# Kernel optimization log

Measured on AMD Instinct MI355X. Metric: run time of the kernel, lower is better.

## Reference

```python
import jax, jax.numpy as jnp
import numpy as np

D = 256   # input_size
H = 512   # hidden_size
A = 4     # alpha_dim
K = 2 * A * A  # output values per input dim (binary=False -> 2 params)


def _masks():
    # MADE sequential-ordering masks, per DART.create_masks
    in_deg = np.arange(D)
    hid_deg = np.arange(H) % (D - 1)
    out_deg = np.arange(D) - 1  # arange(D) % D - 1
    m0 = (hid_deg[:, None] >= in_deg[None, :]).astype(np.float32)   # [H, D]
    mh = (hid_deg[:, None] >= hid_deg[None, :]).astype(np.float32)  # [H, H]
    ml = (out_deg[:, None] >= hid_deg[None, :]).astype(np.float32)  # [D, H]
    # repeat(1, K).view(-1, H): each output-dim row repeated K consecutive times
    ml = np.repeat(ml, K, axis=0)                                    # [D*K, H]
    return jnp.asarray(m0), jnp.asarray(mh), jnp.asarray(ml)


def setup_inputs() -> dict:
    key = jax.random.key(0)
    ks = jax.random.split(key, 10)
    B = 1024
    x = jax.random.normal(ks[0], (B, D), dtype=jnp.float32)
    def lin(k, out_dim, in_dim):
        s = 1.0 / np.sqrt(in_dim)
        kw, kb = jax.random.split(k)
        W = jax.random.uniform(kw, (out_dim, in_dim), jnp.float32, -s, s)
        b = jax.random.uniform(kb, (out_dim,), jnp.float32, -s, s)
        return W, b
    W0, b0 = lin(ks[1], H, D)
    W1, b1 = lin(ks[2], H, H)
    W2, b2 = lin(ks[3], H, H)
    Wout, bout = lin(ks[4], D * K, H)
    # unnormalized_log_p_alpha initialized to log(1/A)
    ulpa = jnp.full((1, D - 1, 1, A), -np.log(A), dtype=jnp.float32)
    return {"x": x, "W0": W0, "b0": b0, "W1": W1, "b1": b1,
            "W2": W2, "b2": b2, "Wout": Wout, "bout": bout, "ulpa": ulpa}


def reference(x, W0, b0, W1, b1, W2, b2, Wout, bout, ulpa):
    m0, mh, ml = _masks()
    B = x.shape[0]
    # masked MLP (MADE)
    h = jax.nn.relu(x @ (m0 * W0).T + b0)
    h = jax.nn.relu(h @ (mh * W1).T + b1)
    h = jax.nn.relu(h @ (mh * W2).T + b2)
    theta = (h @ (ml * Wout).T + bout).reshape(B, D, 2, A, A)
    mu = theta[:, :, 0]                      # [B, D, A, A]
    std = jnp.exp(theta[:, :, 1]) + 0.01     # [B, D, A, A]
    xe = x[:, :, None, None]
    # Normal log-prob
    log_px = -0.5 * jnp.square((xe - mu) / std) - jnp.log(std) - 0.5 * jnp.log(2.0 * jnp.pi)
    # normalized log p(alpha): [1, D-1, 1, A]
    lpa = jax.nn.log_softmax(ulpa, axis=-1)
    joint = log_px[:, :-1] + lpa             # [B, D-1, A, A]
    first = joint[:, 0, 0:1]                 # [B, 1, A]
    inner = jnp.swapaxes(joint[:, 1:], 0, 1)  # [D-2, B, A, A]
    # HMM-style forward recursion: stable log-domain chain matmul via scan
    def step(carry, m):
        # carry: [B, 1, A]; m: [B, A, A]
        new = jax.nn.logsumexp(carry[:, :, :, None] + m[:, None, :, :], axis=-2)
        return new, None
    carry, _ = jax.lax.scan(step, first, inner)
    last = log_px[:, -1, :, 0:1]             # [B, A, 1]
    log_p = jax.nn.logsumexp(carry[:, :, :, None] + last[:, None, :, :], axis=-2)  # [B,1,1]
    return log_p, theta
```

## Files before the change

### kernel.cpp

```cpp
#include <hip/hip_runtime.h>
#include <math.h>

#define Bsz 1024
#define Dd  256
#define Hh  512
#define NOUT 8192

typedef __attribute__((ext_vector_type(8))) short bf8_t;
typedef __attribute__((ext_vector_type(4))) float f4_t;

__device__ inline ushort f2b(float f) {
  union { float f; unsigned u; } c; c.f = f;
  unsigned r = c.u + 0x7fffu + ((c.u >> 16) & 1u);
  return (ushort)(r >> 16);
}

__device__ inline void async16(const ushort* g, ushort* l) {
  __builtin_amdgcn_global_load_lds((const __attribute__((address_space(1))) void*)g,
                                   (__attribute__((address_space(3))) void*)l, 16, 0, 0);
}

__device__ inline int mod255(int v) {
  if (v >= 510) return v - 510;
  if (v >= 255) return v - 255;
  return v;
}

__global__ __launch_bounds__(256) void prep(
    const float* __restrict__ x,  const float* __restrict__ W0,
    const float* __restrict__ W1, const float* __restrict__ W2,
    const float* __restrict__ Wout, const float* __restrict__ ulpa,
    ushort* __restrict__ xb, ushort* __restrict__ w0b, ushort* __restrict__ w1b,
    ushort* __restrict__ w2b, ushort* __restrict__ woutb,
    float* __restrict__ lpa)
{
  const int blk = blockIdx.x, tid = threadIdx.x;
  if (blk == 2496) {
    if (tid < Dd - 1) {
      float v0 = ulpa[tid * 4 + 0], v1 = ulpa[tid * 4 + 1];
      float v2 = ulpa[tid * 4 + 2], v3 = ulpa[tid * 4 + 3];
      float m = fmaxf(fmaxf(v0, v1), fmaxf(v2, v3));
      float s = __expf(v0 - m) + __expf(v1 - m) + __expf(v2 - m) + __expf(v3 - m);
      float l = m + __logf(s);
      lpa[tid * 4 + 0] = v0 - l;
      lpa[tid * 4 + 1] = v1 - l;
      lpa[tid * 4 + 2] = v2 - l;
      lpa[tid * 4 + 3] = v3 - l;
    }
    return;
  }
  const float* src; ushort* dst; int lb, mode;
  if (blk < 128)      { src = x;    dst = xb;    lb = blk;       mode = 0; }
  else if (blk < 192) { src = W0;   dst = w0b;   lb = blk - 128; mode = 1; }
  else if (blk < 320) { src = W1;   dst = w1b;   lb = blk - 192; mode = 2; }
  else if (blk < 448) { src = W2;   dst = w2b;   lb = blk - 320; mode = 2; }
  else                { src = Wout; dst = woutb; lb = blk - 448; mode = 3; }

  const int e = lb * 2048 + tid * 8;
  float4 v0 = *(const float4*)(src + e);
  float4 v1 = *(const float4*)(src + e + 4);
  float vv[8] = {v0.x, v0.y, v0.z, v0.w, v1.x, v1.y, v1.z, v1.w};
  ushort u[8];
  if (mode == 0) {
#pragma unroll
    for (int i = 0; i < 8; i++) u[i] = f2b(vv[i]);
  } else if (mode == 1) {
    int n = e >> 8, k0 = e & 255, nd = mod255(n);
#pragma unroll
    for (int i = 0; i < 8; i++) u[i] = (nd >= k0 + i) ? f2b(vv[i]) : (ushort)0;
  } else if (mode == 2) {
    int n = e >> 9, k0 = e & 511, nd = mod255(n);
#pragma unroll
    for (int i = 0; i < 8; i++) u[i] = (nd >= mod255(k0 + i)) ? f2b(vv[i]) : (ushort)0;
  } else {
    int n = e >> 9, k0 = e & 511, nd = (n >> 5) - 1;
#pragma unroll
    for (int i = 0; i < 8; i++) u[i] = (nd >= mod255(k0 + i)) ? f2b(vv[i]) : (ushort)0;
  }
  *(ushort4*)(dst + e)     = *(ushort4*)&u[0];
  *(ushort4*)(dst + e + 4) = *(ushort4*)&u[4];
}

template<int KD>
__global__ __launch_bounds__(256) void gemm_s(
    const ushort* __restrict__ A, const ushort* __restrict__ W,
    const float* __restrict__ bias, ushort* __restrict__ Ch)
{
  constexpr int NT = KD / 64;
  __shared__ ushort As[3][64 * 64];
  __shared__ ushort Bs[3][32 * 64];
  const int tid = threadIdx.x, lane = tid & 63, wave = tid >> 6;
  const int row0 = blockIdx.y * 64, col0 = blockIdx.x * 32;
  const int fm = lane & 15, qq = lane >> 4;
  const int srow = lane >> 3, qslot = lane & 7;

  f4_t acc[2];
  acc[0] = (f4_t){0.f, 0.f, 0.f, 0.f};
  acc[1] = (f4_t){0.f, 0.f, 0.f, 0.f};

  auto stage = [&](int buf, int kt) {
#pragma unroll
    for (int a = 0; a < 2; a++) {
      int rb = wave * 16 + a * 8;
      int r = rb + srow;
      int q = (qslot - r) & 7;
      async16(A + (size_t)(row0 + r) * KD + kt + q * 8, &As[buf][rb * 64]);
    }
    {
      int rb = wave * 8;
      int r = rb + srow;
      int q = (qslot - r) & 7;
      async16(W + (size_t)(col0 + r) * KD + kt + q * 8, &Bs[buf][rb * 64]);
    }
  };

  stage(0, 0);
  stage(1, 64);

#pragma unroll
  for (int i = 0; i < NT; i++) {
    if (i + 1 < NT) asm volatile("s_waitcnt vmcnt(3)" ::: "memory");
    else            asm volatile("s_waitcnt vmcnt(0)" ::: "memory");
    __builtin_amdgcn_s_barrier();
    asm volatile("" ::: "memory");
    if (i + 2 < NT) stage((i + 2) % 3, (i + 2) * 64);
    const int buf = i % 3;
#pragma unroll
    for (int t = 0; t < 2; t++) {
      int ra = wave * 16 + fm;
      int slota = ((t * 4 + qq) + ra) & 7;
      bf8_t af = *(const bf8_t*)&As[buf][ra * 64 + slota * 8];
#pragma unroll
      for (int j = 0; j < 2; j++) {
        int rb = j * 16 + fm;
        int slot = ((t * 4 + qq) + rb) & 7;
        bf8_t bf = *(const bf8_t*)&Bs[buf][rb * 64 + slot * 8];
        acc[j] = __builtin_amdgcn_mfma_f32_16x16x32_bf16(af, bf, acc[j], 0, 0, 0);
      }
    }
    asm volatile("s_waitcnt lgkmcnt(0)" ::: "memory");
  }

#pragma unroll
  for (int j = 0; j < 2; j++) {
    int col = col0 + j * 16 + fm;
    float bv = bias[col];
    int rbase = row0 + wave * 16 + qq * 4;
#pragma unroll
    for (int r = 0; r < 4; r++) {
      float t = fmaxf(acc[j][r] + bv, 0.0f);
      Ch[(size_t)(rbase + r) * Hh + col] = f2b(t);
    }
  }
}

__global__ __launch_bounds__(256) void gemm_big(
    const ushort* __restrict__ A, const ushort* __restrict__ W,
    const float* __restrict__ bias, float* __restrict__ Cf,
    int M, int N, int Kd)
{
  __shared__ ushort As[2][128 * 64];
  __shared__ ushort Bs[2][128 * 64];
  const int tid = threadIdx.x, lane = tid & 63, wave = tid >> 6;
  const int waveM = wave >> 1, waveN = wave & 1;
  const int row0 = blockIdx.y * 128, col0 = blockIdx.x * 128;
  const int fm = lane & 15, qq = lane >> 4;
  const int srow = lane >> 3, qslot = lane & 7;

  f4_t acc[4][4];
#pragma unroll
  for (int i = 0; i < 4; i++)
#pragma unroll
    for (int j = 0; j < 4; j++) acc[i][j] = (f4_t){0.f, 0.f, 0.f, 0.f};

  auto stage = [&](int buf, int kt) {
#pragma unroll
    for (int p = 0; p < 4; p++) {
      int rb = p * 32 + wave * 8;
      int r = rb + srow;
      int q = (qslot - r) & 7;
      async16(A + (size_t)(row0 + r) * Kd + kt + q * 8, &As[buf][rb * 64]);
    }
#pragma unroll
    for (int p = 0; p < 4; p++) {
      int rb = p * 32 + wave * 8;
      int r = rb + srow;
      int q = (qslot - r) & 7;
      async16(W + (size_t)(col0 + r) * Kd + kt + q * 8, &Bs[buf][rb * 64]);
    }
  };

  stage(0, 0);
  int cur = 0;
  for (int kt = 0; kt < Kd; kt += 64) {
    asm volatile("s_waitcnt vmcnt(0)" ::: "memory");
    __builtin_amdgcn_s_barrier();
    asm volatile("" ::: "memory");
    if (kt + 64 < Kd) stage(cur ^ 1, kt + 64);
#pragma unroll
    for (int t = 0; t < 2; t++) {
      bf8_t af[4], bf[4];
#pragma unroll
      for (int i = 0; i < 4; i++) {
        int r = waveM * 64 + i * 16 + fm;
        int slot = ((t * 4 + qq) + r) & 7;
        af[i] = *(const bf8_t*)&As[cur][r * 64 + slot * 8];
      }
#pragma unroll
      for (int j = 0; j < 4; j++) {
        int r = waveN * 64 + j * 16 + fm;
        int slot = ((t * 4 + qq) + r) & 7;
        bf[j] = *(const bf8_t*)&Bs[cur][r * 64 + slot * 8];
      }
#pragma unroll
      for (int i = 0; i < 4; i++)
#pragma unroll
        for (int j = 0; j < 4; j++)
          acc[i][j] = __builtin_amdgcn_mfma_f32_16x16x32_bf16(af[i], bf[j], acc[i][j], 0, 0, 0);
    }
    asm volatile("s_waitcnt lgkmcnt(0)" ::: "memory");
    cur ^= 1;
  }

#pragma unroll
  for (int j = 0; j < 4; j++) {
    int col = col0 + waveN * 64 + j * 16 + fm;
    float bv = bias[col];
#pragma unroll
    for (int i = 0; i < 4; i++) {
      int rbase = row0 + waveM * 64 + i * 16 + qq * 4;
#pragma unroll
      for (int r = 0; r < 4; r++)
        Cf[(size_t)(rbase + r) * N + col] = acc[i][j][r] + bv;
    }
  }
}

__global__ __launch_bounds__(512) void chain2(
    const float* __restrict__ x, const float* __restrict__ theta,
    const float* __restrict__ lpa, float* __restrict__ logp)
{
  __shared__ float ths[256 * 33];
  __shared__ float xs[256];
  __shared__ float lps[255 * 5];
  __shared__ float TA[32][16];
  __shared__ float TB[16][16];

  const int b = blockIdx.x;
  const int tid = threadIdx.x;
  const float C0 = 0.91893853320467274178f;

  const float4* src = (const float4*)(theta + (size_t)b * NOUT);
#pragma unroll
  for (int it = 0; it < 4; it++) {
    int t = tid + it * 512;
    float4 v = src[t];
    int d = t >> 3, c = (t & 7) * 4;
    float* p = &ths[d * 33 + c];
    p[0] = v.x; p[1] = v.y; p[2] = v.z; p[3] = v.w;
  }
  if (tid < 64) ((float4*)xs)[tid] = ((const float4*)(x + (size_t)b * Dd))[tid];
  if (tid < 255) {
    float4 v = ((const float4*)lpa)[tid];
    float* p = &lps[tid * 5];
    p[0] = v.x; p[1] = v.y; p[2] = v.z; p[3] = v.w;
  }
  __syncthreads();

  const int seg = tid >> 4, e = tid & 15, ii = e >> 2, jj = e & 3;
  const int base = (tid & 63) & ~15;
  const int d0 = 1 + seg * 8;
  const int d1 = min(d0 + 8, Dd - 1);

  auto stepm = [&](int d) -> float {
    float mu = ths[d * 33 + e];
    float ls = ths[d * 33 + 16 + e];
    float s  = __expf(ls) + 0.01f;
    float z  = (xs[d] - mu) * __builtin_amdgcn_rcpf(s);
    return -0.5f * z * z - __logf(s) - C0 + lps[d * 5 + jj];
  };

  float T = stepm(d0);
  for (int d = d0 + 1; d < d1; d++) {
    float m_ = stepm(d);
    float v0 = __shfl(T, base + ii * 4 + 0) + __shfl(m_, base + 0 * 4 + jj);
    float v1 = __shfl(T, base + ii * 4 + 1) + __shfl(m_, base + 1 * 4 + jj);
    float v2 = __shfl(T, base + ii * 4 + 2) + __shfl(m_, base + 2 * 4 + jj);
    float v3 = __shfl(T, base + ii * 4 + 3) + __shfl(m_, base + 3 * 4 + jj);
    float mx = fmaxf(fmaxf(v0, v1), fmaxf(v2, v3));
    float s  = __expf(v0 - mx) + __expf(v1 - mx) + __expf(v2 - mx) + __expf(v3 - mx);
    T = mx + __logf(s);
  }
  TA[seg][e] = T;
  __syncthreads();

  float (*cur)[16] = TA;
  float (*nxt)[16] = TB;
#pragma unroll
  for (int n = 16; n >= 1; n >>= 1) {
    if (tid < n * 16) {
      int p = tid >> 4, ee = tid & 15, i2 = ee >> 2, j2 = ee & 3;
      const float* L = cur[2 * p];
      const float* R = cur[2 * p + 1];
      float v0 = L[i2 * 4 + 0] + R[0 * 4 + j2];
      float v1 = L[i2 * 4 + 1] + R[1 * 4 + j2];
      float v2 = L[i2 * 4 + 2] + R[2 * 4 + j2];
      float v3 = L[i2 * 4 + 3] + R[3 * 4 + j2];
      float mx = fmaxf(fmaxf(v0, v1), fmaxf(v2, v3));
      float ss = __expf(v0 - mx) + __expf(v1 - mx) + __expf(v2 - mx) + __expf(v3 - mx);
      nxt[p][ee] = mx + __logf(ss);
    }
    __syncthreads();
    float (*tmp)[16] = cur; cur = nxt; nxt = tmp;
  }

  if (tid < 16) {
    int i = tid >> 2, j = tid & 3;
    float mu0 = ths[i], ls0 = ths[16 + i];
    float s0 = __expf(ls0) + 0.01f;
    float z0 = (xs[0] - mu0) * __builtin_amdgcn_rcpf(s0);
    float c0 = -0.5f * z0 * z0 - __logf(s0) - C0 + lps[i];
    float muL = ths[255 * 33 + j * 4];
    float lsL = ths[255 * 33 + 16 + j * 4];
    float sL = __expf(lsL) + 0.01f;
    float zL = (xs[255] - muL) * __builtin_amdgcn_rcpf(sL);
    float lL = -0.5f * zL * zL - __logf(sL) - C0;
    float v = c0 + cur[0][tid] + lL;
    float mx = fmaxf(v, __shfl_xor(v, 1));
    mx = fmaxf(mx, __shfl_xor(mx, 2));
    mx = fmaxf(mx, __shfl_xor(mx, 4));
    mx = fmaxf(mx, __shfl_xor(mx, 8));
    float ee = __expf(v - mx);
    ee += __shfl_xor(ee, 1);
    ee += __shfl_xor(ee, 2);
    ee += __shfl_xor(ee, 4);
    ee += __shfl_xor(ee, 8);
    if (tid == 0) logp[b] = mx + __logf(ee);
  }
}

extern "C" void kernel_launch(void* const* d_in, const int* in_sizes, int n_in,
                              void* d_out, int out_size, void* d_ws, size_t ws_size,
                              hipStream_t stream)
{
  const float* x    = (const float*)d_in[0];
  const float* W0   = (const float*)d_in[1];
  const float* b0   = (const float*)d_in[2];
  const float* W1   = (const float*)d_in[3];
  const float* b1   = (const float*)d_in[4];
  const float* W2   = (const float*)d_in[5];
  const float* b2   = (const float*)d_in[6];
  const float* Wout = (const float*)d_in[7];
  const float* bout = (const float*)d_in[8];
  const float* ulpa = (const float*)d_in[9];

  float* out   = (float*)d_out;
  float* logp  = out;
  float* theta = out + Bsz;

  ushort* ws    = (ushort*)d_ws;
  ushort* xb    = ws;
  ushort* w0b   = xb + 262144;
  ushort* w1b   = w0b + 131072;
  ushort* w2b   = w1b + 262144;
  ushort* woutb = w2b + 262144;
  ushort* h0    = woutb + 4194304;
  ushort* h1    = h0 + 524288;
  ushort* h2    = h1 + 524288;
  float*  lpa   = (float*)(h2 + 524288);

  prep<<<2497, 256, 0, stream>>>(x, W0, W1, W2, Wout, ulpa,
                                 xb, w0b, w1b, w2b, woutb, lpa);
  gemm_s<Dd><<<dim3(16, 16), 256, 0, stream>>>(xb, w0b, b0, h0);
  gemm_s<Hh><<<dim3(16, 16), 256, 0, stream>>>(h0, w1b, b1, h1);
  gemm_s<Hh><<<dim3(16, 16), 256, 0, stream>>>(h1, w2b, b2, h2);
  gemm_big<<<dim3(NOUT / 128, Bsz / 128), 256, 0, stream>>>(h2, woutb, bout, theta, Bsz, NOUT, Hh);
  chain2<<<Bsz, 512, 0, stream>>>(x, theta, lpa, logp);
}
```

Measured before the change: 136.1 us.

## Fuse three hidden MLP layers into one kernel with activations kept in LDS

Replaces the three separate gemm_s launches with a single mlp3 kernel. Each of 64 blocks owns 16 batch rows, converts x to bf16 on the fly, and chains all three masked layers through swizzled shared-memory buffers. Only the final layer's activations go to global memory. This removes two kernel launches, the h0/h1 global round trips and the separate x conversion in prep. The cost is far fewer blocks (64 on a large GPU) and weights read directly from global memory without LDS staging, so each block re-reads all weight matrices.

```diff
diff --git a/kernel.cpp b/kernel.cpp
--- a/kernel.cpp
+++ b/kernel.cpp
@@ -27,15 +27,15 @@
 }
 
 __global__ __launch_bounds__(256) void prep(
-    const float* __restrict__ x,  const float* __restrict__ W0,
-    const float* __restrict__ W1, const float* __restrict__ W2,
-    const float* __restrict__ Wout, const float* __restrict__ ulpa,
-    ushort* __restrict__ xb, ushort* __restrict__ w0b, ushort* __restrict__ w1b,
+    const float* __restrict__ W0, const float* __restrict__ W1,
+    const float* __restrict__ W2, const float* __restrict__ Wout,
+    const float* __restrict__ ulpa,
+    ushort* __restrict__ w0b, ushort* __restrict__ w1b,
     ushort* __restrict__ w2b, ushort* __restrict__ woutb,
     float* __restrict__ lpa)
 {
   const int blk = blockIdx.x, tid = threadIdx.x;
-  if (blk == 2496) {
+  if (blk == 2368) {
     if (tid < Dd - 1) {
       float v0 = ulpa[tid * 4 + 0], v1 = ulpa[tid * 4 + 1];
       float v2 = ulpa[tid * 4 + 2], v3 = ulpa[tid * 4 + 3];
@@ -50,21 +50,17 @@
     return;
   }
   const float* src; ushort* dst; int lb, mode;
-  if (blk < 128)      { src = x;    dst = xb;    lb = blk;       mode = 0; }
-  else if (blk < 192) { src = W0;   dst = w0b;   lb = blk - 128; mode = 1; }
-  else if (blk < 320) { src = W1;   dst = w1b;   lb = blk - 192; mode = 2; }
-  else if (blk < 448) { src = W2;   dst = w2b;   lb = blk - 320; mode = 2; }
-  else                { src = Wout; dst = woutb; lb = blk - 448; mode = 3; }
+  if (blk < 64)       { src = W0;   dst = w0b;   lb = blk;       mode = 1; }
+  else if (blk < 192) { src = W1;   dst = w1b;   lb = blk - 64;  mode = 2; }
+  else if (blk < 320) { src = W2;   dst = w2b;   lb = blk - 192; mode = 2; }
+  else                { src = Wout; dst = woutb; lb = blk - 320; mode = 3; }
 
   const int e = lb * 2048 + tid * 8;
   float4 v0 = *(const float4*)(src + e);
   float4 v1 = *(const float4*)(src + e + 4);
   float vv[8] = {v0.x, v0.y, v0.z, v0.w, v1.x, v1.y, v1.z, v1.w};
   ushort u[8];
-  if (mode == 0) {
-#pragma unroll
-    for (int i = 0; i < 8; i++) u[i] = f2b(vv[i]);
-  } else if (mode == 1) {
+  if (mode == 1) {
     int n = e >> 8, k0 = e & 255, nd = mod255(n);
 #pragma unroll
     for (int i = 0; i < 8; i++) u[i] = (nd >= k0 + i) ? f2b(vv[i]) : (ushort)0;
@@ -81,77 +77,74 @@
   *(ushort4*)(dst + e + 4) = *(ushort4*)&u[4];
 }
 
-template<int KD>
-__global__ __launch_bounds__(256) void gemm_s(
-    const ushort* __restrict__ A, const ushort* __restrict__ W,
-    const float* __restrict__ bias, ushort* __restrict__ Ch)
-{
-  constexpr int NT = KD / 64;
-  __shared__ ushort As[3][64 * 64];
-  __shared__ ushort Bs[3][32 * 64];
+template<int KD, bool TO_GLOBAL>
+__device__ __forceinline__ void mlp_layer(
+    const ushort* hin, const ushort* __restrict__ Wg,
+    const float* __restrict__ bias, ushort* hout,
+    int row0, int lane, int wave)
+{
+  const int fm = lane & 15, qq = lane >> 4;
+#pragma unroll
+  for (int ct = 0; ct < 4; ct++) {
+    const int n0 = wave * 64 + ct * 16;
+    const ushort* wrow = Wg + (size_t)(n0 + fm) * KD;
+    f4_t acc = (f4_t){0.f, 0.f, 0.f, 0.f};
+#pragma unroll
+    for (int kt = 0; kt < KD / 64; kt++) {
+#pragma unroll
+      for (int t = 0; t < 2; t++) {
+        const int c = t * 4 + qq;
+        bf8_t af = *(const bf8_t*)&hin[(kt * 16 + fm) * 64 + ((c + fm) & 7) * 8];
+        bf8_t bf = *(const bf8_t*)(wrow + kt * 64 + c * 8);
+        acc = __builtin_amdgcn_mfma_f32_16x16x32_bf16(af, bf, acc, 0, 0, 0);
+      }
+    }
+    const int col = n0 + fm;
+    const float bv = bias[col];
+#pragma unroll
+    for (int r = 0; r < 4; r++) {
+      const int row = qq * 4 + r;
+      float tv = fmaxf(acc[r] + bv, 0.0f);
+      ushort hv = f2b(tv);
+      if (TO_GLOBAL) {
+        hout[(size_t)(row0 + row) * Hh + col] = hv;
+      } else {
+        const int kt2 = col >> 6, q2 = (col >> 3) & 7, w2 = col & 7;
+        hout[(kt2 * 16 + row) * 64 + ((q2 + row) & 7) * 8 + w2] = hv;
+      }
+    }
+  }
+}
+
+__global__ __launch_bounds__(512) void mlp3(
+    const float* __restrict__ x,
+    const ushort* __restrict__ w0b, const float* __restrict__ b0,
+    const ushort* __restrict__ w1b, const float* __restrict__ b1,
+    const ushort* __restrict__ w2b, const float* __restrict__ b2,
+    ushort* __restrict__ h2)
+{
+  __shared__ ushort hA[8 * 16 * 64];
+  __shared__ ushort hB[8 * 16 * 64];
   const int tid = threadIdx.x, lane = tid & 63, wave = tid >> 6;
-  const int row0 = blockIdx.y * 64, col0 = blockIdx.x * 32;
-  const int fm = lane & 15, qq = lane >> 4;
-  const int srow = lane >> 3, qslot = lane & 7;
-
-  f4_t acc[2];
-  acc[0] = (f4_t){0.f, 0.f, 0.f, 0.f};
-  acc[1] = (f4_t){0.f, 0.f, 0.f, 0.f};
-
-  auto stage = [&](int buf, int kt) {
-#pragma unroll
-    for (int a = 0; a < 2; a++) {
-      int rb = wave * 16 + a * 8;
-      int r = rb + srow;
-      int q = (qslot - r) & 7;
-      async16(A + (size_t)(row0 + r) * KD + kt + q * 8, &As[buf][rb * 64]);
-    }
-    {
-      int rb = wave * 8;
-      int r = rb + srow;
-      int q = (qslot - r) & 7;
-      async16(W + (size_t)(col0 + r) * KD + kt + q * 8, &Bs[buf][rb * 64]);
-    }
-  };
-
-  stage(0, 0);
-  stage(1, 64);
-
-#pragma unroll
-  for (int i = 0; i < NT; i++) {
-    if (i + 1 < NT) asm volatile("s_waitcnt vmcnt(3)" ::: "memory");
-    else            asm volatile("s_waitcnt vmcnt(0)" ::: "memory");
-    __builtin_amdgcn_s_barrier();
-    asm volatile("" ::: "memory");
-    if (i + 2 < NT) stage((i + 2) % 3, (i + 2) * 64);
-    const int buf = i % 3;
-#pragma unroll
-    for (int t = 0; t < 2; t++) {
-      int ra = wave * 16 + fm;
-      int slota = ((t * 4 + qq) + ra) & 7;
-      bf8_t af = *(const bf8_t*)&As[buf][ra * 64 + slota * 8];
-#pragma unroll
-      for (int j = 0; j < 2; j++) {
-        int rb = j * 16 + fm;
-        int slot = ((t * 4 + qq) + rb) & 7;
-        bf8_t bf = *(const bf8_t*)&Bs[buf][rb * 64 + slot * 8];
-        acc[j] = __builtin_amdgcn_mfma_f32_16x16x32_bf16(af, bf, acc[j], 0, 0, 0);
-      }
-    }
-    asm volatile("s_waitcnt lgkmcnt(0)" ::: "memory");
-  }
-
-#pragma unroll
-  for (int j = 0; j < 2; j++) {
-    int col = col0 + j * 16 + fm;
-    float bv = bias[col];
-    int rbase = row0 + wave * 16 + qq * 4;
-#pragma unroll
-    for (int r = 0; r < 4; r++) {
-      float t = fmaxf(acc[j][r] + bv, 0.0f);
-      Ch[(size_t)(rbase + r) * Hh + col] = f2b(t);
-    }
-  }
+  const int row0 = blockIdx.x * 16;
+
+#pragma unroll
+  for (int it = 0; it < 2; it++) {
+    int f = it * 512 + tid;
+    int r = f >> 6, k4 = (f & 63) << 2;
+    float4 v = *(const float4*)(x + (size_t)(row0 + r) * Dd + k4);
+    ushort4 u;
+    u.x = f2b(v.x); u.y = f2b(v.y); u.z = f2b(v.z); u.w = f2b(v.w);
+    int t = k4 >> 6, q = (k4 >> 3) & 7, half = (k4 >> 2) & 1;
+    *(ushort4*)&hA[(t * 16 + r) * 64 + ((q + r) & 7) * 8 + half * 4] = u;
+  }
+  __syncthreads();
+
+  mlp_layer<Dd, false>(hA, w0b, b0, hB, row0, lane, wave);
+  __syncthreads();
+  mlp_layer<Hh, false>(hB, w1b, b1, hA, row0, lane, wave);
+  __syncthreads();
+  mlp_layer<Hh, true >(hA, w2b, b2, h2, row0, lane, wave);
 }
 
 __global__ __launch_bounds__(256) void gemm_big(
@@ -359,21 +352,17 @@
   float* theta = out + Bsz;
 
   ushort* ws    = (ushort*)d_ws;
-  ushort* xb    = ws;
-  ushort* w0b   = xb + 262144;
+  ushort* w0b   = ws;
   ushort* w1b   = w0b + 131072;
   ushort* w2b   = w1b + 262144;
   ushort* woutb = w2b + 262144;
-  ushort* h0    = woutb + 4194304;
-  ushort* h1    = h0 + 524288;
-  ushort* h2    = h1 + 524288;
+  ushort* h2    = woutb + 4194304;
   float*  lpa   = (float*)(h2 + 524288);
 
-  prep<<<2497, 256, 0, stream>>>(x, W0, W1, W2, Wout, ulpa,
-                                 xb, w0b, w1b, w2b, woutb, lpa);
-  gemm_s<Dd><<<dim3(16, 16), 256, 0, stream>>>(xb, w0b, b0, h0);
-  gemm_s<Hh><<<dim3(16, 16), 256, 0, stream>>>(h0, w1b, b1, h1);
-  gemm_s<Hh><<<dim3(16, 16), 256, 0, stream>>>(h1, w2b, b2, h2);
-  gemm_big<<<dim3(NOUT / 128, Bsz / 128), 256, 0, stream>>>(h2, woutb, bout, theta, Bsz, NOUT, Hh);
+  prep<<<2369, 256, 0, stream>>>(W0, W1, W2, Wout, ulpa,
+                                 w0b, w1b, w2b, woutb, lpa);
+  mlp3<<<64, 512, 0, stream>>>(x, w0b, b0, w1b, b1, w2b, b2, h2);
+  gemm_big<<<dim3(NOUT / 128, Bsz / 128), 256, 0, stream>>>(
+      h2, woutb, bout, theta, Bsz, NOUT, Hh);
   chain2<<<Bsz, 512, 0, stream>>>(x, theta, lpa, logp);
 }
```

Measured after the change: 162.6 us. +19.5%, slower.

## Shrink hidden-layer GEMM tiles to 32x32 and keep log-prior in registers

Applied to the files above, without the earlier changes.

The three hidden-layer GEMMs now use 32x32 output tiles, one 16x16 MFMA tile per wave, and launch 512 blocks instead of 256 so more of the GPU's compute units are busy. The vmcnt wait is adjusted because each stage now issues one fewer async load. The chain kernel loads its slice of the normalized log-prior directly from global memory into registers, drops the LDS copy, and fully unrolls the per-segment recursion. This trades more blocks and redundant B-tile loads for more parallelism, and per-thread global loads in exchange for less LDS staging.

```diff
diff --git a/kernel.cpp b/kernel.cpp
--- a/kernel.cpp
+++ b/kernel.cpp
@@ -87,21 +87,19 @@
     const float* __restrict__ bias, ushort* __restrict__ Ch)
 {
   constexpr int NT = KD / 64;
-  __shared__ ushort As[3][64 * 64];
+  __shared__ ushort As[3][32 * 64];
   __shared__ ushort Bs[3][32 * 64];
   const int tid = threadIdx.x, lane = tid & 63, wave = tid >> 6;
-  const int row0 = blockIdx.y * 64, col0 = blockIdx.x * 32;
+  const int row0 = blockIdx.y * 32, col0 = blockIdx.x * 32;
+  const int rt = wave >> 1, ct = wave & 1;
   const int fm = lane & 15, qq = lane >> 4;
   const int srow = lane >> 3, qslot = lane & 7;
 
-  f4_t acc[2];
-  acc[0] = (f4_t){0.f, 0.f, 0.f, 0.f};
-  acc[1] = (f4_t){0.f, 0.f, 0.f, 0.f};
+  f4_t acc = (f4_t){0.f, 0.f, 0.f, 0.f};
 
   auto stage = [&](int buf, int kt) {
-#pragma unroll
-    for (int a = 0; a < 2; a++) {
-      int rb = wave * 16 + a * 8;
+    {
+      int rb = wave * 8;
       int r = rb + srow;
       int q = (qslot - r) & 7;
       async16(A + (size_t)(row0 + r) * KD + kt + q * 8, &As[buf][rb * 64]);
@@ -119,7 +117,7 @@
 
 #pragma unroll
   for (int i = 0; i < NT; i++) {
-    if (i + 1 < NT) asm volatile("s_waitcnt vmcnt(3)" ::: "memory");
+    if (i + 1 < NT) asm volatile("s_waitcnt vmcnt(2)" ::: "memory");
     else            asm volatile("s_waitcnt vmcnt(0)" ::: "memory");
     __builtin_amdgcn_s_barrier();
     asm volatile("" ::: "memory");
@@ -127,28 +125,24 @@
     const int buf = i % 3;
 #pragma unroll
     for (int t = 0; t < 2; t++) {
-      int ra = wave * 16 + fm;
+      int ra = rt * 16 + fm;
       int slota = ((t * 4 + qq) + ra) & 7;
       bf8_t af = *(const bf8_t*)&As[buf][ra * 64 + slota * 8];
-#pragma unroll
-      for (int j = 0; j < 2; j++) {
-        int rb = j * 16 + fm;
-        int slot = ((t * 4 + qq) + rb) & 7;
-        bf8_t bf = *(const bf8_t*)&Bs[buf][rb * 64 + slot * 8];
-        acc[j] = __builtin_amdgcn_mfma_f32_16x16x32_bf16(af, bf, acc[j], 0, 0, 0);
-      }
+      int rb = ct * 16 + fm;
+      int slotb = ((t * 4 + qq) + rb) & 7;
+      bf8_t bf = *(const bf8_t*)&Bs[buf][rb * 64 + slotb * 8];
+      acc = __builtin_amdgcn_mfma_f32_16x16x32_bf16(af, bf, acc, 0, 0, 0);
     }
     asm volatile("s_waitcnt lgkmcnt(0)" ::: "memory");
   }
 
-#pragma unroll
-  for (int j = 0; j < 2; j++) {
-    int col = col0 + j * 16 + fm;
+  {
+    int col = col0 + ct * 16 + fm;
     float bv = bias[col];
-    int rbase = row0 + wave * 16 + qq * 4;
+    int rbase = row0 + rt * 16 + qq * 4;
 #pragma unroll
     for (int r = 0; r < 4; r++) {
-      float t = fmaxf(acc[j][r] + bv, 0.0f);
+      float t = fmaxf(acc[r] + bv, 0.0f);
       Ch[(size_t)(rbase + r) * Hh + col] = f2b(t);
     }
   }
@@ -242,13 +236,24 @@
 {
   __shared__ float ths[256 * 33];
   __shared__ float xs[256];
-  __shared__ float lps[255 * 5];
   __shared__ float TA[32][16];
   __shared__ float TB[16][16];
 
   const int b = blockIdx.x;
   const int tid = threadIdx.x;
   const float C0 = 0.91893853320467274178f;
+
+  const int seg = tid >> 4, e = tid & 15, ii = e >> 2, jj = e & 3;
+  const int base = (tid & 63) & ~15;
+  const int d0 = 1 + seg * 8;
+  const int d1 = min(d0 + 8, Dd - 1);
+
+  float lpr[8];
+#pragma unroll
+  for (int k = 0; k < 8; k++) {
+    int d = d0 + k;
+    lpr[k] = lpa[(d <= 254 ? d : 254) * 4 + jj];
+  }
 
   const float4* src = (const float4*)(theta + (size_t)b * NOUT);
 #pragma unroll
@@ -260,36 +265,30 @@
     p[0] = v.x; p[1] = v.y; p[2] = v.z; p[3] = v.w;
   }
   if (tid < 64) ((float4*)xs)[tid] = ((const float4*)(x + (size_t)b * Dd))[tid];
-  if (tid < 255) {
-    float4 v = ((const float4*)lpa)[tid];
-    float* p = &lps[tid * 5];
-    p[0] = v.x; p[1] = v.y; p[2] = v.z; p[3] = v.w;
-  }
   __syncthreads();
 
-  const int seg = tid >> 4, e = tid & 15, ii = e >> 2, jj = e & 3;
-  const int base = (tid & 63) & ~15;
-  const int d0 = 1 + seg * 8;
-  const int d1 = min(d0 + 8, Dd - 1);
-
-  auto stepm = [&](int d) -> float {
+  auto stepm = [&](int d, float lp) -> float {
     float mu = ths[d * 33 + e];
     float ls = ths[d * 33 + 16 + e];
     float s  = __expf(ls) + 0.01f;
     float z  = (xs[d] - mu) * __builtin_amdgcn_rcpf(s);
-    return -0.5f * z * z - __logf(s) - C0 + lps[d * 5 + jj];
+    return -0.5f * z * z - __logf(s) - C0 + lp;
   };
 
-  float T = stepm(d0);
-  for (int d = d0 + 1; d < d1; d++) {
-    float m_ = stepm(d);
-    float v0 = __shfl(T, base + ii * 4 + 0) + __shfl(m_, base + 0 * 4 + jj);
-    float v1 = __shfl(T, base + ii * 4 + 1) + __shfl(m_, base + 1 * 4 + jj);
-    float v2 = __shfl(T, base + ii * 4 + 2) + __shfl(m_, base + 2 * 4 + jj);
-    float v3 = __shfl(T, base + ii * 4 + 3) + __shfl(m_, base + 3 * 4 + jj);
-    float mx = fmaxf(fmaxf(v0, v1), fmaxf(v2, v3));
-    float s  = __expf(v0 - mx) + __expf(v1 - mx) + __expf(v2 - mx) + __expf(v3 - mx);
-    T = mx + __logf(s);
+  float T = stepm(d0, lpr[0]);
+#pragma unroll
+  for (int k = 1; k < 8; k++) {
+    int d = d0 + k;
+    if (d < d1) {
+      float m_ = stepm(d, lpr[k]);
+      float v0 = __shfl(T, base + ii * 4 + 0) + __shfl(m_, base + 0 * 4 + jj);
+      float v1 = __shfl(T, base + ii * 4 + 1) + __shfl(m_, base + 1 * 4 + jj);
+      float v2 = __shfl(T, base + ii * 4 + 2) + __shfl(m_, base + 2 * 4 + jj);
+      float v3 = __shfl(T, base + ii * 4 + 3) + __shfl(m_, base + 3 * 4 + jj);
+      float mx = fmaxf(fmaxf(v0, v1), fmaxf(v2, v3));
+      float s  = __expf(v0 - mx) + __expf(v1 - mx) + __expf(v2 - mx) + __expf(v3 - mx);
+      T = mx + __logf(s);
+    }
   }
   TA[seg][e] = T;
   __syncthreads();
@@ -319,7 +318,7 @@
     float mu0 = ths[i], ls0 = ths[16 + i];
     float s0 = __expf(ls0) + 0.01f;
     float z0 = (xs[0] - mu0) * __builtin_amdgcn_rcpf(s0);
-    float c0 = -0.5f * z0 * z0 - __logf(s0) - C0 + lps[i];
+    float c0 = -0.5f * z0 * z0 - __logf(s0) - C0 + lpa[i];
     float muL = ths[255 * 33 + j * 4];
     float lsL = ths[255 * 33 + 16 + j * 4];
     float sL = __expf(lsL) + 0.01f;
@@ -371,9 +370,9 @@
 
   prep<<<2497, 256, 0, stream>>>(x, W0, W1, W2, Wout, ulpa,
                                  xb, w0b, w1b, w2b, woutb, lpa);
-  gemm_s<Dd><<<dim3(16, 16), 256, 0, stream>>>(xb, w0b, b0, h0);
-  gemm_s<Hh><<<dim3(16, 16), 256, 0, stream>>>(h0, w1b, b1, h1);
-  gemm_s<Hh><<<dim3(16, 16), 256, 0, stream>>>(h1, w2b, b2, h2);
+  gemm_s<Dd><<<dim3(16, 32), 256, 0, stream>>>(xb, w0b, b0, h0);
+  gemm_s<Hh><<<dim3(16, 32), 256, 0, stream>>>(h0, w1b, b1, h1);
+  gemm_s<Hh><<<dim3(16, 32), 256, 0, stream>>>(h1, w2b, b2, h2);
   gemm_big<<<dim3(NOUT / 128, Bsz / 128), 256, 0, stream>>>(h2, woutb, bout, theta, Bsz, NOUT, Hh);
   chain2<<<Bsz, 512, 0, stream>>>(x, theta, lpa, logp);
 }
```

Result: no change. 137.6 us (+1.1%).
